# Kernel tuning notes

Hardware: AMD Instinct MI355X
Metric: run time of the kernel (lower is better)

The kernel has to match this reference:

```python
import jax, jax.numpy as jnp
import numpy as np

B, NV, NQ, NA = 128, 100, 14, 10
V_DIM, Q_DIM, A_DIM = 2048, 1024, 1024
H_DIM, RANK, HD, G = 512, 32, 16, 2  # HD = H_DIM // RANK, G = glimpse


def setup_inputs() -> dict:
    key = jax.random.key(0)
    ks = jax.random.split(key, 16)
    s = 0.05
    return {
        "v": jax.random.normal(ks[0], (B, NV, V_DIM), jnp.float32),
        "q": jax.random.normal(ks[1], (B, NQ, Q_DIM), jnp.float32),
        "a": jax.random.normal(ks[2], (B, NA, A_DIM), jnp.float32),
        # tucker projections (FCNet = Linear + ReLU; dropout identity at eval)
        "Wv": jax.random.normal(ks[3], (H_DIM, V_DIM), jnp.float32) * s,
        "bv": jnp.zeros((H_DIM,), jnp.float32),
        "Wq": jax.random.normal(ks[4], (H_DIM, Q_DIM), jnp.float32) * s,
        "bq": jnp.zeros((H_DIM,), jnp.float32),
        "Wa": jax.random.normal(ks[5], (H_DIM, A_DIM), jnp.float32) * s,
        "ba": jnp.zeros((H_DIM,), jnp.float32),
        # rank-wise projection nets, stacked over rank: [rank, HD, H_DIM]
        "Wvr": jax.random.normal(ks[6], (RANK, HD, H_DIM), jnp.float32) * s,
        "bvr": jnp.zeros((RANK, HD), jnp.float32),
        "Wqr": jax.random.normal(ks[7], (RANK, HD, H_DIM), jnp.float32) * s,
        "bqr": jnp.zeros((RANK, HD), jnp.float32),
        "War": jax.random.normal(ks[8], (RANK, HD, H_DIM), jnp.float32) * s,
        "bar": jnp.zeros((RANK, HD), jnp.float32),
        # Tucker core T_g with h_out squeezed: [rank, hv, hq, ha, glimpse]
        "T": jax.random.normal(ks[9], (RANK, HD, HD, HD, G), jnp.float32),
    }


def reference(v, q, a, Wv, bv, Wq, bq, Wa, ba, Wvr, bvr, Wqr, bqr, War, bar, T):
    relu = jax.nn.relu
    # modality tucker projections: [B, N, H_DIM]
    vt = relu(jnp.einsum('bnd,hd->bnh', v, Wv) + bv)
    qt = relu(jnp.einsum('bnd,hd->bnh', q, Wq) + bq)
    at = relu(jnp.einsum('bnd,hd->bnh', a, Wa) + ba)
    # rank-wise FCNets, batched over rank: [B, rank, N, HD]
    v_ = relu(jnp.einsum('bnh,rch->brnc', vt, Wvr) + bvr[None, :, None, :])
    q_ = relu(jnp.einsum('bnh,rch->brnc', qt, Wqr) + bqr[None, :, None, :])
    a_ = relu(jnp.einsum('bnh,rch->brnc', at, War) + bar[None, :, None, :])
    # 6-way Tucker contraction, summed over rank: [B, NV, NQ, NA, G]
    f_emb = jnp.einsum('rijkg,bnvi,bnqj,bnak->bvqag', T, v_, q_, a_,
                       optimize=True)
    return f_emb
```

## Files before the change

kernel.cpp:

```cpp
#include <hip/hip_runtime.h>
#include <cstddef>
#include <cstdint>

#define B_    128
#define NV_   100
#define NQ_   14
#define NA_   10
#define HDIM  512
#define RANK_ 32
#define HD_   16
#define G_    2

typedef __bf16 bf16x8 __attribute__((ext_vector_type(8)));
typedef float  f32x4  __attribute__((ext_vector_type(4)));
union Frag { uint4 u; bf16x8 v; };

__device__ __forceinline__ unsigned int f2bf(float f) {
  unsigned int u = __float_as_uint(f);
  u = (u + 0x7FFFu + ((u >> 16) & 1u)) >> 16;
  return u & 0xFFFFu;
}

__global__ __launch_bounds__(256) void cvt_kernel(
    const float* __restrict__ s0, const float* __restrict__ s1,
    const float* __restrict__ s2, const float* __restrict__ s3,
    const float* __restrict__ s4, const float* __restrict__ s5,
    const float* __restrict__ s6, const float* __restrict__ s7,
    unsigned short* __restrict__ dst)
{
  const int pref[8] = {896, 1536, 2048, 2304, 2560, 2688, 2816, 2944};
  const float* srcs[8] = {s0, s1, s2, s3, s4, s5, s6, s7};
  const int blk = blockIdx.x;
  int seg = 0;
  #pragma unroll
  for (int i = 0; i < 7; ++i) if (blk >= pref[i]) seg = i + 1;
  const int base_chunk = seg ? pref[seg - 1] : 0;
  const size_t loc = (size_t)(blk - base_chunk) * 2048 + threadIdx.x * 8;
  const float* s = srcs[seg] + loc;
  float4 f0 = *(const float4*)s;
  float4 f1 = *(const float4*)(s + 4);
  ushort4 o0, o1;
  o0.x = f2bf(f0.x); o0.y = f2bf(f0.y); o0.z = f2bf(f0.z); o0.w = f2bf(f0.w);
  o1.x = f2bf(f1.x); o1.y = f2bf(f1.y); o1.z = f2bf(f1.z); o1.w = f2bf(f1.w);
  unsigned short* d = dst + (size_t)blk * 2048 + threadIdx.x * 8;
  *(ushort4*)d = o0;
  *(ushort4*)(d + 4) = o1;
}

__global__ __launch_bounds__(256) void l1_gemm(
    const float* __restrict__ v,
    const unsigned short* __restrict__ qb, const unsigned short* __restrict__ ab,
    const unsigned short* __restrict__ Wvb, const unsigned short* __restrict__ Wqb,
    const unsigned short* __restrict__ Wab,
    const float* __restrict__ bv, const float* __restrict__ bq,
    const float* __restrict__ ba,
    unsigned short* __restrict__ vtb, unsigned short* __restrict__ qtb,
    unsigned short* __restrict__ atb)
{
  __shared__ __align__(16) unsigned short As[4096];
  __shared__ __align__(16) unsigned short Bs[4096];
  const int bx = blockIdx.x;
  int grp, gx, gy, K;
  const unsigned short *A16 = qb, *W;
  const float* bias;
  unsigned short* C;
  if (bx < 400)      { grp = 0; gx = bx & 3; gy = bx >> 2;           W = Wvb; bias = bv; C = vtb; K = 2048; }
  else if (bx < 456) { grp = 1; int lo = bx - 400; gx = lo & 3; gy = lo >> 2; A16 = qb; W = Wqb; bias = bq; C = qtb; K = 1024; }
  else               { grp = 2; int lo = bx - 456; gx = lo & 3; gy = lo >> 2; A16 = ab; W = Wab; bias = ba; C = atb; K = 1024; }
  const int bn = gx * 128, bm = gy * 128;
  const int t = threadIdx.x;
  const int w = t >> 6, l = t & 63;
  const int wm = (w >> 1) * 64, wn = (w & 1) * 64;
  const int rr = l >> 2, ko = (l & 3) * 8;

  f32x4 acc[4][4];
  #pragma unroll
  for (int i = 0; i < 4; ++i)
    #pragma unroll
    for (int j = 0; j < 4; ++j) acc[i][j] = f32x4{0.f, 0.f, 0.f, 0.f};

  if (grp == 0) {
    const int row = t >> 1, half = t & 1;
    for (int k0 = 0; k0 < 2048; k0 += 32) {
      const float* src = v + (size_t)(bm + row) * 2048 + k0 + half * 16;
      float4 f0 = *(const float4*)(src + 0);
      float4 f1 = *(const float4*)(src + 4);
      float4 f2 = *(const float4*)(src + 8);
      float4 f3 = *(const float4*)(src + 12);
      #pragma unroll
      for (int c2 = 0; c2 < 2; ++c2) {
        const int c = w * 2 + c2;
        const unsigned short* gpB = W + (size_t)(bn + c * 16 + rr) * 2048 + k0 + ko;
        __builtin_amdgcn_global_load_lds(
            (const __attribute__((address_space(1))) void*)gpB,
            (__attribute__((address_space(3))) void*)&Bs[c * 512], 16, 0, 0);
      }
      uint4 p0, p1;
      p0.x = f2bf(f0.x) | (f2bf(f0.y) << 16);
      p0.y = f2bf(f0.z) | (f2bf(f0.w) << 16);
      p0.z = f2bf(f1.x) | (f2bf(f1.y) << 16);
      p0.w = f2bf(f1.z) | (f2bf(f1.w) << 16);
      p1.x = f2bf(f2.x) | (f2bf(f2.y) << 16);
      p1.y = f2bf(f2.z) | (f2bf(f2.w) << 16);
      p1.z = f2bf(f3.x) | (f2bf(f3.y) << 16);
      p1.w = f2bf(f3.z) | (f2bf(f3.w) << 16);
      *(uint4*)&As[row * 32 + half * 16]     = p0;
      *(uint4*)&As[row * 32 + half * 16 + 8] = p1;
      __syncthreads();
      Frag fa[4], fb[4];
      #pragma unroll
      for (int i = 0; i < 4; ++i)
        fa[i].u = *(const uint4*)&As[(wm + 16 * i + (l & 15)) * 32 + (l >> 4) * 8];
      #pragma unroll
      for (int j = 0; j < 4; ++j)
        fb[j].u = *(const uint4*)&Bs[(wn + 16 * j + (l & 15)) * 32 + (l >> 4) * 8];
      #pragma unroll
      for (int i = 0; i < 4; ++i)
        #pragma unroll
        for (int j = 0; j < 4; ++j)
          acc[i][j] = __builtin_amdgcn_mfma_f32_16x16x32_bf16(fa[i].v, fb[j].v, acc[i][j], 0, 0, 0);
      __syncthreads();
    }
  } else {
    for (int k0 = 0; k0 < K; k0 += 32) {
      #pragma unroll
      for (int c2 = 0; c2 < 2; ++c2) {
        const int c = w * 2 + c2;
        const unsigned short* gpA = A16 + (size_t)(bm + c * 16 + rr) * K + k0 + ko;
        const unsigned short* gpB = W   + (size_t)(bn + c * 16 + rr) * K + k0 + ko;
        __builtin_amdgcn_global_load_lds(
            (const __attribute__((address_space(1))) void*)gpA,
            (__attribute__((address_space(3))) void*)&As[c * 512], 16, 0, 0);
        __builtin_amdgcn_global_load_lds(
            (const __attribute__((address_space(1))) void*)gpB,
            (__attribute__((address_space(3))) void*)&Bs[c * 512], 16, 0, 0);
      }
      __syncthreads();
      Frag fa[4], fb[4];
      #pragma unroll
      for (int i = 0; i < 4; ++i)
        fa[i].u = *(const uint4*)&As[(wm + 16 * i + (l & 15)) * 32 + (l >> 4) * 8];
      #pragma unroll
      for (int j = 0; j < 4; ++j)
        fb[j].u = *(const uint4*)&Bs[(wn + 16 * j + (l & 15)) * 32 + (l >> 4) * 8];
      #pragma unroll
      for (int i = 0; i < 4; ++i)
        #pragma unroll
        for (int j = 0; j < 4; ++j)
          acc[i][j] = __builtin_amdgcn_mfma_f32_16x16x32_bf16(fa[i].v, fb[j].v, acc[i][j], 0, 0, 0);
      __syncthreads();
    }
  }

  const int q4 = (l >> 4) * 4, cl = l & 15;
  #pragma unroll
  for (int i = 0; i < 4; ++i)
    #pragma unroll
    for (int j = 0; j < 4; ++j) {
      const int col = bn + wn + 16 * j + cl;
      const float bs = bias[col];
      #pragma unroll
      for (int r = 0; r < 4; ++r) {
        const int row = bm + wm + 16 * i + q4 + r;
        float o = fmaxf(acc[i][j][r] + bs, 0.f);
        C[(size_t)row * 512 + col] = (unsigned short)f2bf(o);
      }
    }
}

__global__ __launch_bounds__(256) void l2_gemm(
    const unsigned short* __restrict__ vtb, const unsigned short* __restrict__ qtb,
    const unsigned short* __restrict__ atb,
    const unsigned short* __restrict__ Wvrb, const unsigned short* __restrict__ Wqrb,
    const unsigned short* __restrict__ Warb,
    const float* __restrict__ bvr, const float* __restrict__ bqr,
    const float* __restrict__ bar,
    unsigned short* __restrict__ vrb, float* __restrict__ q_r, float* __restrict__ a_r)
{
  __shared__ __align__(16) unsigned short As[4096];
  __shared__ __align__(16) unsigned short Bs[4096];
  const int bx = blockIdx.x;
  int grp, gx, gy;
  const unsigned short *A16, *W;
  const float* bias;
  if (bx < 400)      { grp = 0; gx = bx & 3; gy = bx >> 2;           A16 = vtb; W = Wvrb; bias = bvr; }
  else if (bx < 456) { grp = 1; int lo = bx - 400; gx = lo & 3; gy = lo >> 2; A16 = qtb; W = Wqrb; bias = bqr; }
  else               { grp = 2; int lo = bx - 456; gx = lo & 3; gy = lo >> 2; A16 = atb; W = Warb; bias = bar; }
  const int bn = gx * 128, bm = gy * 128;
  const int t = threadIdx.x;
  const int w = t >> 6, l = t & 63;
  const int wm = (w >> 1) * 64, wn = (w & 1) * 64;
  const int rr = l >> 2, ko = (l & 3) * 8;

  f32x4 acc[4][4];
  #pragma unroll
  for (int i = 0; i < 4; ++i)
    #pragma unroll
    for (int j = 0; j < 4; ++j) acc[i][j] = f32x4{0.f, 0.f, 0.f, 0.f};

  for (int k0 = 0; k0 < 512; k0 += 32) {
    #pragma unroll
    for (int c2 = 0; c2 < 2; ++c2) {
      const int c = w * 2 + c2;
      const unsigned short* gpA = A16 + (size_t)(bm + c * 16 + rr) * 512 + k0 + ko;
      const unsigned short* gpB = W   + (size_t)(bn + c * 16 + rr) * 512 + k0 + ko;
      __builtin_amdgcn_global_load_lds(
          (const __attribute__((address_space(1))) void*)gpA,
          (__attribute__((address_space(3))) void*)&As[c * 512], 16, 0, 0);
      __builtin_amdgcn_global_load_lds(
          (const __attribute__((address_space(1))) void*)gpB,
          (__attribute__((address_space(3))) void*)&Bs[c * 512], 16, 0, 0);
    }
    __syncthreads();
    Frag fa[4], fb[4];
    #pragma unroll
    for (int i = 0; i < 4; ++i)
      fa[i].u = *(const uint4*)&As[(wm + 16 * i + (l & 15)) * 32 + (l >> 4) * 8];
    #pragma unroll
    for (int j = 0; j < 4; ++j)
      fb[j].u = *(const uint4*)&Bs[(wn + 16 * j + (l & 15)) * 32 + (l >> 4) * 8];
    #pragma unroll
    for (int i = 0; i < 4; ++i)
      #pragma unroll
      for (int j = 0; j < 4; ++j)
        acc[i][j] = __builtin_amdgcn_mfma_f32_16x16x32_bf16(fa[i].v, fb[j].v, acc[i][j], 0, 0, 0);
    __syncthreads();
  }

  const int q4 = (l >> 4) * 4, cl = l & 15;
  #pragma unroll
  for (int i = 0; i < 4; ++i)
    #pragma unroll
    for (int j = 0; j < 4; ++j) {
      const int col = bn + wn + 16 * j + cl;
      const float bs = bias[col];
      #pragma unroll
      for (int r = 0; r < 4; ++r) {
        const int row = bm + wm + 16 * i + q4 + r;
        float o = fmaxf(acc[i][j][r] + bs, 0.f);
        if (grp == 0)      vrb[(size_t)row * 512 + col] = (unsigned short)f2bf(o);
        else if (grp == 1) q_r[(size_t)row * 512 + col] = o;
        else               a_r[(size_t)row * 512 + col] = o;
      }
    }
}

__global__ void tsum_kernel(const float* __restrict__ T, float* __restrict__ Tsum)
{
  const int idx = blockIdx.x * 256 + threadIdx.x;
  float s = 0.f;
  #pragma unroll
  for (int r = 0; r < RANK_; ++r) s += T[r * 8192 + idx];
  Tsum[idx] = s;
}

__global__ __launch_bounds__(256) void build_w_kernel(
    const float* __restrict__ q_, const float* __restrict__ a_,
    const float* __restrict__ Tsum, unsigned short* __restrict__ WmatT)
{
  const int n = blockIdx.x, b = blockIdx.y, t = threadIdx.x;
  __shared__ float Ts[8192];
  __shared__ float U[14 * 544];

  #pragma unroll
  for (int s = 0; s < 8; ++s)
    ((float4*)Ts)[s * 256 + t] = ((const float4*)Tsum)[s * 256 + t];
  __syncthreads();

  {
    const int i = t >> 4, k = t & 15;
    float acc0[NQ_], acc1[NQ_];
    #pragma unroll
    for (int q = 0; q < NQ_; ++q) { acc0[q] = 0.f; acc1[q] = 0.f; }
    const float* qbase = q_ + (size_t)b * NQ_ * HDIM + n * 16;
    #pragma unroll
    for (int j = 0; j < 16; ++j) {
      float2 ts = *(const float2*)&Ts[i * 512 + j * 32 + k * 2];
      #pragma unroll
      for (int q = 0; q < NQ_; ++q) {
        float qv = qbase[q * HDIM + j];
        acc0[q] += ts.x * qv;
        acc1[q] += ts.y * qv;
      }
    }
    #pragma unroll
    for (int q = 0; q < NQ_; ++q) {
      float2 uu; uu.x = acc0[q]; uu.y = acc1[q];
      *(float2*)&U[q * 544 + i * 34 + k * 2] = uu;
    }
  }
  __syncthreads();

  if ((t >> 4) < NQ_) {
    const int q = t >> 4, i = t & 15;
    float acc0[NA_], acc1[NA_];
    #pragma unroll
    for (int a = 0; a < NA_; ++a) { acc0[a] = 0.f; acc1[a] = 0.f; }
    const float* abase = a_ + (size_t)b * NA_ * HDIM + n * 16;
    #pragma unroll
    for (int k = 0; k < 16; ++k) {
      float2 uu = *(const float2*)&U[q * 544 + i * 34 + k * 2];
      #pragma unroll
      for (int a = 0; a < NA_; ++a) {
        float av = abase[a * HDIM + k];
        acc0[a] += uu.x * av;
        acc1[a] += uu.y * av;
      }
    }
    unsigned short* wb = WmatT + (size_t)b * 320 * 512 + (n * 16 + i);
    #pragma unroll
    for (int a = 0; a < NA_; ++a) {
      wb[(size_t)((q * 10 + a) * 2 + 0) * 512] = (unsigned short)f2bf(acc0[a]);
      wb[(size_t)((q * 10 + a) * 2 + 1) * 512] = (unsigned short)f2bf(acc1[a]);
    }
  }
}

__global__ __launch_bounds__(512) void final_mfma(
    const unsigned short* __restrict__ Vrb, const unsigned short* __restrict__ WmatT,
    float* __restrict__ out)
{
  __shared__ __align__(16) unsigned short As[128 * 32];
  __shared__ __align__(16) unsigned short Bs[160 * 32];
  const int b  = blockIdx.y;
  const int n0 = blockIdx.x * 160;
  const int t = threadIdx.x;
  const int w = t >> 6, l = t & 63;
  const int wm = (w >> 1) * 32;
  const int wn = (w & 1) * 80;

  f32x4 acc[2][5];
  #pragma unroll
  for (int mi = 0; mi < 2; ++mi)
    #pragma unroll
    for (int nj = 0; nj < 5; ++nj) acc[mi][nj] = f32x4{0.f, 0.f, 0.f, 0.f};

  const unsigned short* Wb = WmatT + (size_t)b * 320 * 512;

  for (int k0 = 0; k0 < 512; k0 += 32) {
    {
      int grow = b * NV_ + w * 16 + (l >> 2);
      if (grow > B_ * NV_ - 1) grow = B_ * NV_ - 1;
      const unsigned short* src = Vrb + (size_t)grow * HDIM + k0 + (l & 3) * 8;
      __builtin_amdgcn_global_load_lds(
          (const __attribute__((address_space(1))) void*)src,
          (__attribute__((address_space(3))) void*)&As[w * 512], 16, 0, 0);
    }
    #pragma unroll
    for (int c = 0; c < 2; ++c) {
      const int base = c * 512 + w * 64;
      if (base < 640) {
        const int li = base + l;
        const int nrow = li >> 2, ko2 = (li & 3) * 8;
        const unsigned short* src = Wb + (size_t)(n0 + nrow) * 512 + k0 + ko2;
        __builtin_amdgcn_global_load_lds(
            (const __attribute__((address_space(1))) void*)src,
            (__attribute__((address_space(3))) void*)&Bs[base * 8], 16, 0, 0);
      }
    }
    __syncthreads();

    Frag fa[2], fb[5];
    #pragma unroll
    for (int mi = 0; mi < 2; ++mi)
      fa[mi].u = *(const uint4*)&As[(wm + mi * 16 + (l & 15)) * 32 + (l >> 4) * 8];
    #pragma unroll
    for (int nj = 0; nj < 5; ++nj)
      fb[nj].u = *(const uint4*)&Bs[(wn + nj * 16 + (l & 15)) * 32 + (l >> 4) * 8];
    #pragma unroll
    for (int mi = 0; mi < 2; ++mi)
      #pragma unroll
      for (int nj = 0; nj < 5; ++nj)
        acc[mi][nj] = __builtin_amdgcn_mfma_f32_16x16x32_bf16(fa[mi].v, fb[nj].v, acc[mi][nj], 0, 0, 0);
    __syncthreads();
  }

  #pragma unroll
  for (int mi = 0; mi < 2; ++mi)
    #pragma unroll
    for (int nj = 0; nj < 5; ++nj) {
      const int col = n0 + wn + nj * 16 + (l & 15);
      if (col < 280) {
        #pragma unroll
        for (int r = 0; r < 4; ++r) {
          const int row = wm + mi * 16 + (l >> 4) * 4 + r;
          if (row < NV_)
            out[((size_t)b * NV_ + row) * 280 + col] = acc[mi][nj][r];
        }
      }
    }
}

extern "C" void kernel_launch(void* const* d_in, const int* in_sizes, int n_in,
                              void* d_out, int out_size, void* d_ws, size_t ws_size,
                              hipStream_t stream)
{
  const float* v   = (const float*)d_in[0];
  const float* q   = (const float*)d_in[1];
  const float* a   = (const float*)d_in[2];
  const float* Wv  = (const float*)d_in[3];
  const float* bv  = (const float*)d_in[4];
  const float* Wq  = (const float*)d_in[5];
  const float* bq  = (const float*)d_in[6];
  const float* Wa  = (const float*)d_in[7];
  const float* ba  = (const float*)d_in[8];
  const float* Wvr = (const float*)d_in[9];
  const float* bvr = (const float*)d_in[10];
  const float* Wqr = (const float*)d_in[11];
  const float* bqr = (const float*)d_in[12];
  const float* War = (const float*)d_in[13];
  const float* bar = (const float*)d_in[14];
  const float* T   = (const float*)d_in[15];

  unsigned short* wsu = (unsigned short*)d_ws;
  float* wsf = (float*)d_ws;

  unsigned short* WmatT = wsu;
  unsigned short* qb    = wsu;
  unsigned short* ab    = wsu + 1835008;
  unsigned short* Wvb   = wsu + 3145728;
  unsigned short* Wqb   = wsu + 4194304;
  unsigned short* Wab   = wsu + 4718592;
  unsigned short* Wvrb  = wsu + 5242880;
  unsigned short* Wqrb  = wsu + 5505024;
  unsigned short* Warb  = wsu + 5767168;
  unsigned short* vtb   = wsu + 20971520;
  unsigned short* qtb   = wsu + 27525120;
  unsigned short* atb   = wsu + 28442624;
  unsigned short* vrb   = wsu + 29097984;
  float* q_r  = wsf + 17825792;
  float* a_r  = wsf + 18743296;
  float* Tsum = wsf + 19398656;

  cvt_kernel<<<2944, 256, 0, stream>>>(q, a, Wv, Wq, Wa, Wvr, Wqr, War, wsu);

  l1_gemm<<<496, 256, 0, stream>>>(v, qb, ab, Wvb, Wqb, Wab, bv, bq, ba,
                                   vtb, qtb, atb);
  l2_gemm<<<496, 256, 0, stream>>>(vtb, qtb, atb, Wvrb, Wqrb, Warb,
                                   bvr, bqr, bar, vrb, q_r, a_r);

  tsum_kernel<<<32, 256, 0, stream>>>(T, Tsum);
  build_w_kernel<<<dim3(32, 128), 256, 0, stream>>>(q_r, a_r, Tsum, WmatT);
  final_mfma<<<dim3(2, 128), 512, 0, stream>>>(vrb, WmatT, (float*)d_out);
}
```

Baseline: 364.7 us.

## Halve GEMM M-tiles to double block count and add XCD-aware block mapping

```diff
diff --git a/kernel.cpp b/kernel.cpp
--- a/kernel.cpp
+++ b/kernel.cpp
@@ -57,36 +57,42 @@
     unsigned short* __restrict__ vtb, unsigned short* __restrict__ qtb,
     unsigned short* __restrict__ atb)
 {
-  __shared__ __align__(16) unsigned short As[4096];
+  __shared__ __align__(16) unsigned short As[2048];
   __shared__ __align__(16) unsigned short Bs[4096];
   const int bx = blockIdx.x;
   int grp, gx, gy, K;
   const unsigned short *A16 = qb, *W;
   const float* bias;
   unsigned short* C;
-  if (bx < 400)      { grp = 0; gx = bx & 3; gy = bx >> 2;           W = Wvb; bias = bv; C = vtb; K = 2048; }
-  else if (bx < 456) { grp = 1; int lo = bx - 400; gx = lo & 3; gy = lo >> 2; A16 = qb; W = Wqb; bias = bq; C = qtb; K = 1024; }
-  else               { grp = 2; int lo = bx - 456; gx = lo & 3; gy = lo >> 2; A16 = ab; W = Wab; bias = ba; C = atb; K = 1024; }
-  const int bn = gx * 128, bm = gy * 128;
+  if (bx < 800) {
+    grp = 0; const int xcd = bx & 7; const int j = bx >> 3;
+    gy = xcd * 25 + (j >> 2); gx = j & 3;
+    W = Wvb; bias = bv; C = vtb; K = 2048;
+  } else if (bx < 912) {
+    grp = 1; const int lo = bx - 800; gy = lo >> 2; gx = lo & 3;
+    A16 = qb; W = Wqb; bias = bq; C = qtb; K = 1024;
+  } else {
+    grp = 2; const int lo = bx - 912; gy = lo >> 2; gx = lo & 3;
+    A16 = ab; W = Wab; bias = ba; C = atb; K = 1024;
+  }
+  const int bm = gy * 64, bn = gx * 128;
   const int t = threadIdx.x;
   const int w = t >> 6, l = t & 63;
-  const int wm = (w >> 1) * 64, wn = (w & 1) * 64;
+  const int wm = (w >> 1) * 32, wn = (w & 1) * 64;
   const int rr = l >> 2, ko = (l & 3) * 8;
 
-  f32x4 acc[4][4];
-  #pragma unroll
-  for (int i = 0; i < 4; ++i)
+  f32x4 acc[2][4];
+  #pragma unroll
+  for (int i = 0; i < 2; ++i)
     #pragma unroll
     for (int j = 0; j < 4; ++j) acc[i][j] = f32x4{0.f, 0.f, 0.f, 0.f};
 
   if (grp == 0) {
-    const int row = t >> 1, half = t & 1;
+    const int row = t >> 2, koff = (t & 3) * 8;
     for (int k0 = 0; k0 < 2048; k0 += 32) {
-      const float* src = v + (size_t)(bm + row) * 2048 + k0 + half * 16;
+      const float* src = v + (size_t)(bm + row) * 2048 + k0 + koff;
       float4 f0 = *(const float4*)(src + 0);
       float4 f1 = *(const float4*)(src + 4);
-      float4 f2 = *(const float4*)(src + 8);
-      float4 f3 = *(const float4*)(src + 12);
       #pragma unroll
       for (int c2 = 0; c2 < 2; ++c2) {
         const int c = w * 2 + c2;
@@ -95,27 +101,22 @@
             (const __attribute__((address_space(1))) void*)gpB,
             (__attribute__((address_space(3))) void*)&Bs[c * 512], 16, 0, 0);
       }
-      uint4 p0, p1;
-      p0.x = f2bf(f0.x) | (f2bf(f0.y) << 16);
-      p0.y = f2bf(f0.z) | (f2bf(f0.w) << 16);
-      p0.z = f2bf(f1.x) | (f2bf(f1.y) << 16);
-      p0.w = f2bf(f1.z) | (f2bf(f1.w) << 16);
-      p1.x = f2bf(f2.x) | (f2bf(f2.y) << 16);
-      p1.y = f2bf(f2.z) | (f2bf(f2.w) << 16);
-      p1.z = f2bf(f3.x) | (f2bf(f3.y) << 16);
-      p1.w = f2bf(f3.z) | (f2bf(f3.w) << 16);
-      *(uint4*)&As[row * 32 + half * 16]     = p0;
-      *(uint4*)&As[row * 32 + half * 16 + 8] = p1;
+      uint4 p;
+      p.x = f2bf(f0.x) | (f2bf(f0.y) << 16);
+      p.y = f2bf(f0.z) | (f2bf(f0.w) << 16);
+      p.z = f2bf(f1.x) | (f2bf(f1.y) << 16);
+      p.w = f2bf(f1.z) | (f2bf(f1.w) << 16);
+      *(uint4*)&As[row * 32 + koff] = p;
       __syncthreads();
-      Frag fa[4], fb[4];
-      #pragma unroll
-      for (int i = 0; i < 4; ++i)
+      Frag fa[2], fb[4];
+      #pragma unroll
+      for (int i = 0; i < 2; ++i)
         fa[i].u = *(const uint4*)&As[(wm + 16 * i + (l & 15)) * 32 + (l >> 4) * 8];
       #pragma unroll
       for (int j = 0; j < 4; ++j)
         fb[j].u = *(const uint4*)&Bs[(wn + 16 * j + (l & 15)) * 32 + (l >> 4) * 8];
       #pragma unroll
-      for (int i = 0; i < 4; ++i)
+      for (int i = 0; i < 2; ++i)
         #pragma unroll
         for (int j = 0; j < 4; ++j)
           acc[i][j] = __builtin_amdgcn_mfma_f32_16x16x32_bf16(fa[i].v, fb[j].v, acc[i][j], 0, 0, 0);
@@ -123,28 +124,30 @@
     }
   } else {
     for (int k0 = 0; k0 < K; k0 += 32) {
+      {
+        const unsigned short* gpA = A16 + (size_t)(bm + w * 16 + rr) * K + k0 + ko;
+        __builtin_amdgcn_global_load_lds(
+            (const __attribute__((address_space(1))) void*)gpA,
+            (__attribute__((address_space(3))) void*)&As[w * 512], 16, 0, 0);
+      }
       #pragma unroll
       for (int c2 = 0; c2 < 2; ++c2) {
         const int c = w * 2 + c2;
-        const unsigned short* gpA = A16 + (size_t)(bm + c * 16 + rr) * K + k0 + ko;
-        const unsigned short* gpB = W   + (size_t)(bn + c * 16 + rr) * K + k0 + ko;
-        __builtin_amdgcn_global_load_lds(
-            (const __attribute__((address_space(1))) void*)gpA,
-            (__attribute__((address_space(3))) void*)&As[c * 512], 16, 0, 0);
+        const unsigned short* gpB = W + (size_t)(bn + c * 16 + rr) * K + k0 + ko;
         __builtin_amdgcn_global_load_lds(
             (const __attribute__((address_space(1))) void*)gpB,
             (__attribute__((address_space(3))) void*)&Bs[c * 512], 16, 0, 0);
       }
       __syncthreads();
-      Frag fa[4], fb[4];
-      #pragma unroll
-      for (int i = 0; i < 4; ++i)
+      Frag fa[2], fb[4];
+      #pragma unroll
+      for (int i = 0; i < 2; ++i)
         fa[i].u = *(const uint4*)&As[(wm + 16 * i + (l & 15)) * 32 + (l >> 4) * 8];
       #pragma unroll
       for (int j = 0; j < 4; ++j)
         fb[j].u = *(const uint4*)&Bs[(wn + 16 * j + (l & 15)) * 32 + (l >> 4) * 8];
       #pragma unroll
-      for (int i = 0; i < 4; ++i)
+      for (int i = 0; i < 2; ++i)
         #pragma unroll
         for (int j = 0; j < 4; ++j)
           acc[i][j] = __builtin_amdgcn_mfma_f32_16x16x32_bf16(fa[i].v, fb[j].v, acc[i][j], 0, 0, 0);
@@ -154,7 +157,7 @@
 
   const int q4 = (l >> 4) * 4, cl = l & 15;
   #pragma unroll
-  for (int i = 0; i < 4; ++i)
+  for (int i = 0; i < 2; ++i)
     #pragma unroll
     for (int j = 0; j < 4; ++j) {
       const int col = bn + wn + 16 * j + cl;
@@ -177,50 +180,60 @@
     const float* __restrict__ bar,
     unsigned short* __restrict__ vrb, float* __restrict__ q_r, float* __restrict__ a_r)
 {
-  __shared__ __align__(16) unsigned short As[4096];
+  __shared__ __align__(16) unsigned short As[2048];
   __shared__ __align__(16) unsigned short Bs[4096];
   const int bx = blockIdx.x;
   int grp, gx, gy;
   const unsigned short *A16, *W;
   const float* bias;
-  if (bx < 400)      { grp = 0; gx = bx & 3; gy = bx >> 2;           A16 = vtb; W = Wvrb; bias = bvr; }
-  else if (bx < 456) { grp = 1; int lo = bx - 400; gx = lo & 3; gy = lo >> 2; A16 = qtb; W = Wqrb; bias = bqr; }
-  else               { grp = 2; int lo = bx - 456; gx = lo & 3; gy = lo >> 2; A16 = atb; W = Warb; bias = bar; }
-  const int bn = gx * 128, bm = gy * 128;
+  if (bx < 800) {
+    grp = 0; const int xcd = bx & 7; const int j = bx >> 3;
+    gy = xcd * 25 + (j >> 2); gx = j & 3;
+    A16 = vtb; W = Wvrb; bias = bvr;
+  } else if (bx < 912) {
+    grp = 1; const int lo = bx - 800; gy = lo >> 2; gx = lo & 3;
+    A16 = qtb; W = Wqrb; bias = bqr;
+  } else {
+    grp = 2; const int lo = bx - 912; gy = lo >> 2; gx = lo & 3;
+    A16 = atb; W = Warb; bias = bar;
+  }
+  const int bm = gy * 64, bn = gx * 128;
   const int t = threadIdx.x;
   const int w = t >> 6, l = t & 63;
-  const int wm = (w >> 1) * 64, wn = (w & 1) * 64;
+  const int wm = (w >> 1) * 32, wn = (w & 1) * 64;
   const int rr = l >> 2, ko = (l & 3) * 8;
 
-  f32x4 acc[4][4];
-  #pragma unroll
-  for (int i = 0; i < 4; ++i)
+  f32x4 acc[2][4];
+  #pragma unroll
+  for (int i = 0; i < 2; ++i)
     #pragma unroll
     for (int j = 0; j < 4; ++j) acc[i][j] = f32x4{0.f, 0.f, 0.f, 0.f};
 
   for (int k0 = 0; k0 < 512; k0 += 32) {
+    {
+      const unsigned short* gpA = A16 + (size_t)(bm + w * 16 + rr) * 512 + k0 + ko;
+      __builtin_amdgcn_global_load_lds(
+          (const __attribute__((address_space(1))) void*)gpA,
+          (__attribute__((address_space(3))) void*)&As[w * 512], 16, 0, 0);
+    }
     #pragma unroll
     for (int c2 = 0; c2 < 2; ++c2) {
       const int c = w * 2 + c2;
-      const unsigned short* gpA = A16 + (size_t)(bm + c * 16 + rr) * 512 + k0 + ko;
-      const unsigned short* gpB = W   + (size_t)(bn + c * 16 + rr) * 512 + k0 + ko;
-      __builtin_amdgcn_global_load_lds(
-          (const __attribute__((address_space(1))) void*)gpA,
-          (__attribute__((address_space(3))) void*)&As[c * 512], 16, 0, 0);
+      const unsigned short* gpB = W + (size_t)(bn + c * 16 + rr) * 512 + k0 + ko;
       __builtin_amdgcn_global_load_lds(
           (const __attribute__((address_space(1))) void*)gpB,
           (__attribute__((address_space(3))) void*)&Bs[c * 512], 16, 0, 0);
     }
     __syncthreads();
-    Frag fa[4], fb[4];
-    #pragma unroll
-    for (int i = 0; i < 4; ++i)
+    Frag fa[2], fb[4];
+    #pragma unroll
+    for (int i = 0; i < 2; ++i)
       fa[i].u = *(const uint4*)&As[(wm + 16 * i + (l & 15)) * 32 + (l >> 4) * 8];
     #pragma unroll
     for (int j = 0; j < 4; ++j)
       fb[j].u = *(const uint4*)&Bs[(wn + 16 * j + (l & 15)) * 32 + (l >> 4) * 8];
     #pragma unroll
-    for (int i = 0; i < 4; ++i)
+    for (int i = 0; i < 2; ++i)
       #pragma unroll
       for (int j = 0; j < 4; ++j)
         acc[i][j] = __builtin_amdgcn_mfma_f32_16x16x32_bf16(fa[i].v, fb[j].v, acc[i][j], 0, 0, 0);
@@ -229,7 +242,7 @@
 
   const int q4 = (l >> 4) * 4, cl = l & 15;
   #pragma unroll
-  for (int i = 0; i < 4; ++i)
+  for (int i = 0; i < 2; ++i)
     #pragma unroll
     for (int j = 0; j < 4; ++j) {
       const int col = bn + wn + 16 * j + cl;
@@ -316,14 +329,15 @@
   }
 }
 
-__global__ __launch_bounds__(512) void final_mfma(
+__global__ __launch_bounds__(256) void final_mfma(
     const unsigned short* __restrict__ Vrb, const unsigned short* __restrict__ WmatT,
     float* __restrict__ out)
 {
-  __shared__ __align__(16) unsigned short As[128 * 32];
-  __shared__ __align__(16) unsigned short Bs[160 * 32];
+  __shared__ __align__(16) unsigned short As[2048];
+  __shared__ __align__(16) unsigned short Bs[5120];
   const int b  = blockIdx.y;
-  const int n0 = blockIdx.x * 160;
+  const int mh = blockIdx.x >> 1;
+  const int n0 = (blockIdx.x & 1) * 160;
   const int t = threadIdx.x;
   const int w = t >> 6, l = t & 63;
   const int wm = (w >> 1) * 32;
@@ -339,7 +353,7 @@
 
   for (int k0 = 0; k0 < 512; k0 += 32) {
     {
-      int grow = b * NV_ + w * 16 + (l >> 2);
+      int grow = b * NV_ + mh * 64 + w * 16 + (l >> 2);
       if (grow > B_ * NV_ - 1) grow = B_ * NV_ - 1;
       const unsigned short* src = Vrb + (size_t)grow * HDIM + k0 + (l & 3) * 8;
       __builtin_amdgcn_global_load_lds(
@@ -347,8 +361,8 @@
           (__attribute__((address_space(3))) void*)&As[w * 512], 16, 0, 0);
     }
     #pragma unroll
-    for (int c = 0; c < 2; ++c) {
-      const int base = c * 512 + w * 64;
+    for (int c = 0; c < 3; ++c) {
+      const int base = c * 256 + w * 64;
       if (base < 640) {
         const int li = base + l;
         const int nrow = li >> 2, ko2 = (li & 3) * 8;
@@ -383,7 +397,7 @@
       if (col < 280) {
         #pragma unroll
         for (int r = 0; r < 4; ++r) {
-          const int row = wm + mi * 16 + (l >> 4) * 4 + r;
+          const int row = mh * 64 + wm + mi * 16 + (l >> 4) * 4 + r;
           if (row < NV_)
             out[((size_t)b * NV_ + row) * 280 + col] = acc[mi][nj][r];
         }
@@ -434,12 +448,12 @@
 
   cvt_kernel<<<2944, 256, 0, stream>>>(q, a, Wv, Wq, Wa, Wvr, Wqr, War, wsu);
 
-  l1_gemm<<<496, 256, 0, stream>>>(v, qb, ab, Wvb, Wqb, Wab, bv, bq, ba,
+  l1_gemm<<<992, 256, 0, stream>>>(v, qb, ab, Wvb, Wqb, Wab, bv, bq, ba,
                                    vtb, qtb, atb);
-  l2_gemm<<<496, 256, 0, stream>>>(vtb, qtb, atb, Wvrb, Wqrb, Warb,
+  l2_gemm<<<992, 256, 0, stream>>>(vtb, qtb, atb, Wvrb, Wqrb, Warb,
                                    bvr, bqr, bar, vrb, q_r, a_r);
 
   tsum_kernel<<<32, 256, 0, stream>>>(T, Tsum);
   build_w_kernel<<<dim3(32, 128), 256, 0, stream>>>(q_r, a_r, Tsum, WmatT);
-  final_mfma<<<dim3(2, 128), 512, 0, stream>>>(vrb, WmatT, (float*)d_out);
-}
+  final_mfma<<<dim3(4, 128), 256, 0, stream>>>(vrb, WmatT, (float*)d_out);
+}
```

Measured after the change: 354.5 us. 1.03x faster.
